# Performance work log

Measured on AMD Instinct MI355X. Metric: run time of the kernel, lower is better.

## Reference

```python
import jax, jax.numpy as jnp
import numpy as np

VOCAB = 100000
EMBED = 300
BATCH = 131072
NEG = 10


def setup_inputs() -> dict:
    key = jax.random.key(0)
    k1, k2, k3, k4, k5 = jax.random.split(key, 5)
    center_words = jax.random.randint(k1, (BATCH,), 0, VOCAB)
    context_words = jax.random.randint(k2, (BATCH,), 0, VOCAB)
    neg_samples = jax.random.randint(k3, (BATCH, NEG), 0, VOCAB)
    in_embed = jax.random.normal(k4, (VOCAB, EMBED), dtype=jnp.float32)
    out_embed = jax.random.normal(k5, (VOCAB, EMBED), dtype=jnp.float32)
    return {
        "center_words": center_words,
        "context_words": context_words,
        "neg_samples": neg_samples,
        "in_embed": in_embed,
        "out_embed": out_embed,
    }


def reference(center_words, context_words, neg_samples, in_embed, out_embed):
    center_e = in_embed[center_words]          # [B, D]
    context_e = out_embed[context_words]       # [B, D]
    neg_e = out_embed[neg_samples]             # [B, K, D]
    pos_scores = jnp.sum(center_e * context_e, axis=1)            # [B]
    neg_scores = jnp.einsum("bkd,bd->bk", neg_e, center_e)        # [B, K]
    pos_loss = jax.nn.log_sigmoid(pos_scores)                      # [B]
    neg_loss = jnp.sum(jax.nn.log_sigmoid(-neg_scores), axis=1)   # [B]
    return -jnp.mean(pos_loss + neg_loss)
```

## Files before the change

### kernel.cpp

```cpp
#include <hip/hip_runtime.h>
#include <math.h>

#define VOCABN 100000
#define EMBED 300
#define BATCH 131072
#define NEG 10
#define RQ 19
#define NWORDS (VOCABN * EMBED)

typedef float float2v __attribute__((ext_vector_type(2)));


template <bool HI>
__device__ __forceinline__ float2v cvt2(unsigned int w) {
    return __builtin_amdgcn_cvt_pk_f32_fp8((int)w, HI);
}
template <bool HI>
__device__ __forceinline__ unsigned int pk2(unsigned int old, float a, float b) {
    return (unsigned int)__builtin_amdgcn_cvt_pk_fp8_f32(a, b, (int)old, HI);
}

__device__ __forceinline__ float dqf(const float* c, uint4 q) {
    float2v p;
    float s = 0.0f;
    p = cvt2<false>(q.x); s += c[0]  * p.x + c[1]  * p.y;
    p = cvt2<true >(q.x); s += c[2]  * p.x + c[3]  * p.y;
    p = cvt2<false>(q.y); s += c[4]  * p.x + c[5]  * p.y;
    p = cvt2<true >(q.y); s += c[6]  * p.x + c[7]  * p.y;
    p = cvt2<false>(q.z); s += c[8]  * p.x + c[9]  * p.y;
    p = cvt2<true >(q.z); s += c[10] * p.x + c[11] * p.y;
    p = cvt2<false>(q.w); s += c[12] * p.x + c[13] * p.y;
    p = cvt2<true >(q.w); s += c[14] * p.x + c[15] * p.y;
    return s;
}

__device__ __forceinline__ void unp16(uint4 q, float* f) {
    float2v p;
    p = cvt2<false>(q.x); f[0]  = p.x; f[1]  = p.y;
    p = cvt2<true >(q.x); f[2]  = p.x; f[3]  = p.y;
    p = cvt2<false>(q.y); f[4]  = p.x; f[5]  = p.y;
    p = cvt2<true >(q.y); f[6]  = p.x; f[7]  = p.y;
    p = cvt2<false>(q.z); f[8]  = p.x; f[9]  = p.y;
    p = cvt2<true >(q.z); f[10] = p.x; f[11] = p.y;
    p = cvt2<false>(q.w); f[12] = p.x; f[13] = p.y;
    p = cvt2<true >(q.w); f[14] = p.x; f[15] = p.y;
}


__device__ __forceinline__ float dot4(const float4 a, const float4 b) {
    return a.x * b.x + a.y * b.y + a.z * b.z + a.w * b.w;
}

__device__ __forceinline__ float lsig(float x) {
    float ax = fabsf(x);
    return fminf(x, 0.0f) - __logf(1.0f + __expf(-ax));
}

__device__ __forceinline__ float reduce16(float v) {
    v += __shfl_xor(v, 1);
    v += __shfl_xor(v, 2);
    v += __shfl_xor(v, 4);
    v += __shfl_xor(v, 8);
    return v;
}

__global__ void sgns_zero_acc(double* acc) { *acc = 0.0; }

__global__ void sgns_finalize(const double* __restrict__ acc, float* __restrict__ out) {
    *out = (float)(-(*acc) / (double)BATCH);
}


__global__ __launch_bounds__(256) void cvt_fp8(const float* __restrict__ src,
                                               uint4* __restrict__ dst, int nrows) {
    const int total = nrows * RQ;
    const int stride = gridDim.x * blockDim.x;
    for (int i = blockIdx.x * blockDim.x + threadIdx.x; i < total; i += stride) {
        int r = i / RQ;
        int q = i - r * RQ;
        const float4* s = reinterpret_cast<const float4*>(src + (size_t)r * EMBED + q * 16);
        float4 a = s[0], b = s[1], c = s[2];
        float4 d = make_float4(0.f, 0.f, 0.f, 0.f);
        if (q != RQ - 1) d = s[3];
        uint4 o;
        unsigned int w;
        w = pk2<false>(0, a.x, a.y); o.x = pk2<true>(w, a.z, a.w);
        w = pk2<false>(0, b.x, b.y); o.y = pk2<true>(w, b.z, b.w);
        w = pk2<false>(0, c.x, c.y); o.z = pk2<true>(w, c.z, c.w);
        w = pk2<false>(0, d.x, d.y); o.w = pk2<true>(w, d.z, d.w);
        dst[i] = o;
    }
}


__global__ __launch_bounds__(256) void sgns_fp8(
    const int* __restrict__ center_words,
    const int* __restrict__ context_words,
    const int* __restrict__ neg_samples,
    const uint4* __restrict__ inQ,
    const uint4* __restrict__ outQ,
    double* __restrict__ acc)
{
    const int lane = threadIdx.x & 15;
    const int group = (blockIdx.x * blockDim.x + threadIdx.x) >> 4;
    const int nGroups = (gridDim.x * blockDim.x) >> 4;
    const int tl = (lane < 3) ? lane : 0;
    const float tmask = (lane < 3) ? 1.0f : 0.0f;

    float tsum = 0.0f;

    for (int b = group; b < BATCH; b += nGroups) {
        const int cw = center_words[b];
        const int xw = context_words[b];
        const int2* np = reinterpret_cast<const int2*>(neg_samples + (size_t)b * NEG);
        int2 q0 = np[0], q1 = np[1], q2 = np[2], q3 = np[3], q4 = np[4];
        int idx[11] = {xw, q0.x, q0.y, q1.x, q1.y, q2.x, q2.y, q3.x, q3.y, q4.x, q4.y};

        const uint4* cp = inQ + (size_t)cw * RQ;
        uint4 cm = cp[lane];
        uint4 ct = cp[16 + tl];
        float cf[32];
        unp16(cm, cf);
        unp16(ct, cf + 16);
        #pragma unroll
        for (int j = 16; j < 32; ++j) cf[j] *= tmask;

        float part[11];
        uint4 bm[3], bt[3];
        {
            const uint4* p0 = outQ + (size_t)idx[0] * RQ;
            bm[0] = p0[lane]; bt[0] = p0[16 + tl];
            const uint4* p1 = outQ + (size_t)idx[1] * RQ;
            bm[1] = p1[lane]; bt[1] = p1[16 + tl];
        }
        #pragma unroll
        for (int j = 0; j < 11; ++j) {
            if (j + 2 < 11) {
                const uint4* p = outQ + (size_t)idx[j + 2] * RQ;
                bm[(j + 2) % 3] = p[lane];
                bt[(j + 2) % 3] = p[16 + tl];
            }
            part[j] = dqf(cf, bm[j % 3]) + dqf(cf + 16, bt[j % 3]);
        }

        #pragma unroll
        for (int j = 0; j < 11; ++j) part[j] = reduce16(part[j]);

        float loss = lsig(part[0]);
        #pragma unroll
        for (int j = 1; j < 11; ++j) loss += lsig(-part[j]);

        tsum += (lane == 0) ? loss : 0.0f;
    }

    float w = tsum;
    #pragma unroll
    for (int m = 1; m < 64; m <<= 1) w += __shfl_xor(w, m);

    __shared__ double ssum[4];
    const int wid = threadIdx.x >> 6;
    if ((threadIdx.x & 63) == 0) ssum[wid] = (double)w;
    __syncthreads();
    if (threadIdx.x == 0) {
        atomicAdd(acc, ssum[0] + ssum[1] + ssum[2] + ssum[3]);
    }
}


__global__ __launch_bounds__(256) void sgns_f32(
    const int* __restrict__ center_words,
    const int* __restrict__ context_words,
    const int* __restrict__ neg_samples,
    const float* __restrict__ in_embed,
    const float* __restrict__ out_embed,
    double* __restrict__ acc)
{
    const int lane = threadIdx.x & 15;
    const int group = (blockIdx.x * blockDim.x + threadIdx.x) >> 4;
    const int nGroups = (gridDim.x * blockDim.x) >> 4;

    const float4* inE = reinterpret_cast<const float4*>(in_embed);
    const float4* outE = reinterpret_cast<const float4*>(out_embed);
    const int RU = EMBED / 4;
    const int TAIL = RU - 64;

    float tsum = 0.0f;

    for (int b = group; b < BATCH; b += nGroups) {
        const int c = center_words[b];
        const int ctx = context_words[b];

        const float4* crow = inE + (size_t)c * RU;
        float4 c0 = crow[lane + 0];
        float4 c1 = crow[lane + 16];
        float4 c2 = crow[lane + 32];
        float4 c3 = crow[lane + 48];
        float4 c4 = make_float4(0.f, 0.f, 0.f, 0.f);
        if (lane < TAIL) c4 = crow[lane + 64];

        const float4* xrow = outE + (size_t)ctx * RU;
        float p = dot4(c0, xrow[lane + 0])
                + dot4(c1, xrow[lane + 16])
                + dot4(c2, xrow[lane + 32])
                + dot4(c3, xrow[lane + 48]);
        if (lane < TAIL) p += dot4(c4, xrow[lane + 64]);
        p = reduce16(p);

        float loss = lsig(p);

        #pragma unroll
        for (int k = 0; k < NEG; ++k) {
            const int nk = neg_samples[b * NEG + k];
            const float4* nrow = outE + (size_t)nk * RU;
            float s = dot4(c0, nrow[lane + 0])
                    + dot4(c1, nrow[lane + 16])
                    + dot4(c2, nrow[lane + 32])
                    + dot4(c3, nrow[lane + 48]);
            if (lane < TAIL) s += dot4(c4, nrow[lane + 64]);
            s = reduce16(s);
            loss += lsig(-s);
        }

        tsum += (lane == 0) ? loss : 0.0f;
    }

    float w = tsum;
    #pragma unroll
    for (int m = 1; m < 64; m <<= 1) w += __shfl_xor(w, m);

    __shared__ double ssum[4];
    const int wid = threadIdx.x >> 6;
    if ((threadIdx.x & 63) == 0) ssum[wid] = (double)w;
    __syncthreads();
    if (threadIdx.x == 0) {
        atomicAdd(acc, ssum[0] + ssum[1] + ssum[2] + ssum[3]);
    }
}


extern "C" void kernel_launch(void* const* d_in, const int* in_sizes, int n_in,
                              void* d_out, int out_size, void* d_ws, size_t ws_size,
                              hipStream_t stream) {
    const int* center = (const int*)d_in[0];
    const int* context = (const int*)d_in[1];
    const int* negs = (const int*)d_in[2];
    const float* inE = (const float*)d_in[3];
    const float* outE = (const float*)d_in[4];
    float* out = (float*)d_out;
    double* acc = (double*)d_ws;

    sgns_zero_acc<<<1, 1, 0, stream>>>(acc);

    const size_t TBL_BYTES = (size_t)VOCABN * RQ * 16;
    const size_t need = 256 + 2 * TBL_BYTES;

    if (ws_size >= need) {
        uint4* inQ = (uint4*)((char*)d_ws + 256);
        uint4* outQ = (uint4*)((char*)d_ws + 256 + TBL_BYTES);
        cvt_fp8<<<4096, 256, 0, stream>>>(inE, inQ, VOCABN);
        cvt_fp8<<<4096, 256, 0, stream>>>(outE, outQ, VOCABN);
        sgns_fp8<<<2048, 256, 0, stream>>>(center, context, negs,
                                           (const uint4*)inQ, (const uint4*)outQ, acc);
    } else {
        sgns_f32<<<2048, 256, 0, stream>>>(center, context, negs, inE, outE, acc);
    }

    sgns_finalize<<<1, 1, 0, stream>>>(acc, out);
}
```

Baseline: 153.8 us.

## Merge fp8 table conversions, pad rows to 20 chunks, use packed float2 math

Fuses the two table-to-fp8 conversion launches into one kernel using nontemporal loads, and pads each quantized row to 20 16-byte chunks so row starts align and the tail read uses four lanes. The dot product is rewritten to use packed float2 multiply-accumulate. The aim is to cut launch overhead, cache pollution during conversion, and ALU work in the gather-dot loop. The workspace need grows because of the padding.

```diff
diff --git a/kernel.cpp b/kernel.cpp
--- a/kernel.cpp
+++ b/kernel.cpp
@@ -5,10 +5,10 @@
 #define EMBED 300
 #define BATCH 131072
 #define NEG 10
-#define RQ 19
-#define NWORDS (VOCABN * EMBED)
+#define RQ 20
 
 typedef float float2v __attribute__((ext_vector_type(2)));
+typedef float float4v __attribute__((ext_vector_type(4)));
 
 
 template <bool HI>
@@ -20,30 +20,27 @@
     return (unsigned int)__builtin_amdgcn_cvt_pk_fp8_f32(a, b, (int)old, HI);
 }
 
-__device__ __forceinline__ float dqf(const float* c, uint4 q) {
-    float2v p;
-    float s = 0.0f;
-    p = cvt2<false>(q.x); s += c[0]  * p.x + c[1]  * p.y;
-    p = cvt2<true >(q.x); s += c[2]  * p.x + c[3]  * p.y;
-    p = cvt2<false>(q.y); s += c[4]  * p.x + c[5]  * p.y;
-    p = cvt2<true >(q.y); s += c[6]  * p.x + c[7]  * p.y;
-    p = cvt2<false>(q.z); s += c[8]  * p.x + c[9]  * p.y;
-    p = cvt2<true >(q.z); s += c[10] * p.x + c[11] * p.y;
-    p = cvt2<false>(q.w); s += c[12] * p.x + c[13] * p.y;
-    p = cvt2<true >(q.w); s += c[14] * p.x + c[15] * p.y;
-    return s;
-}
-
-__device__ __forceinline__ void unp16(uint4 q, float* f) {
-    float2v p;
-    p = cvt2<false>(q.x); f[0]  = p.x; f[1]  = p.y;
-    p = cvt2<true >(q.x); f[2]  = p.x; f[3]  = p.y;
-    p = cvt2<false>(q.y); f[4]  = p.x; f[5]  = p.y;
-    p = cvt2<true >(q.y); f[6]  = p.x; f[7]  = p.y;
-    p = cvt2<false>(q.z); f[8]  = p.x; f[9]  = p.y;
-    p = cvt2<true >(q.z); f[10] = p.x; f[11] = p.y;
-    p = cvt2<false>(q.w); f[12] = p.x; f[13] = p.y;
-    p = cvt2<true >(q.w); f[14] = p.x; f[15] = p.y;
+__device__ __forceinline__ float2v dq8(const float2v* c, uint4 q, float2v acc) {
+    acc += c[0] * cvt2<false>(q.x);
+    acc += c[1] * cvt2<true >(q.x);
+    acc += c[2] * cvt2<false>(q.y);
+    acc += c[3] * cvt2<true >(q.y);
+    acc += c[4] * cvt2<false>(q.z);
+    acc += c[5] * cvt2<true >(q.z);
+    acc += c[6] * cvt2<false>(q.w);
+    acc += c[7] * cvt2<true >(q.w);
+    return acc;
+}
+
+__device__ __forceinline__ void unp8(uint4 q, float2v* f) {
+    f[0] = cvt2<false>(q.x);
+    f[1] = cvt2<true >(q.x);
+    f[2] = cvt2<false>(q.y);
+    f[3] = cvt2<true >(q.y);
+    f[4] = cvt2<false>(q.z);
+    f[5] = cvt2<true >(q.z);
+    f[6] = cvt2<false>(q.w);
+    f[7] = cvt2<true >(q.w);
 }
 
 
@@ -71,24 +68,36 @@
 }
 
 
-__global__ __launch_bounds__(256) void cvt_fp8(const float* __restrict__ src,
-                                               uint4* __restrict__ dst, int nrows) {
-    const int total = nrows * RQ;
+__global__ __launch_bounds__(256) void cvt_fp8_all(
+    const float* __restrict__ srcA, const float* __restrict__ srcB,
+    uint4* __restrict__ dstA, uint4* __restrict__ dstB)
+{
+    const int T = VOCABN * RQ;
+    const int total = 2 * T;
     const int stride = gridDim.x * blockDim.x;
     for (int i = blockIdx.x * blockDim.x + threadIdx.x; i < total; i += stride) {
-        int r = i / RQ;
-        int q = i - r * RQ;
-        const float4* s = reinterpret_cast<const float4*>(src + (size_t)r * EMBED + q * 16);
-        float4 a = s[0], b = s[1], c = s[2];
-        float4 d = make_float4(0.f, 0.f, 0.f, 0.f);
-        if (q != RQ - 1) d = s[3];
-        uint4 o;
-        unsigned int w;
-        w = pk2<false>(0, a.x, a.y); o.x = pk2<true>(w, a.z, a.w);
-        w = pk2<false>(0, b.x, b.y); o.y = pk2<true>(w, b.z, b.w);
-        w = pk2<false>(0, c.x, c.y); o.z = pk2<true>(w, c.z, c.w);
-        w = pk2<false>(0, d.x, d.y); o.w = pk2<true>(w, d.z, d.w);
-        dst[i] = o;
+        const int t = (i >= T);
+        const int j = i - t * T;
+        const int r = j / RQ;
+        const int q = j - r * RQ;
+        const float* src = t ? srcB : srcA;
+        uint4* dst = t ? dstB : dstA;
+
+        uint4 o = make_uint4(0u, 0u, 0u, 0u);
+        if (q < 19) {
+            const float4v* s = reinterpret_cast<const float4v*>(src + (size_t)r * EMBED + q * 16);
+            float4v a = __builtin_nontemporal_load(s);
+            float4v b = __builtin_nontemporal_load(s + 1);
+            float4v c = __builtin_nontemporal_load(s + 2);
+            float4v d = {0.f, 0.f, 0.f, 0.f};
+            if (q < 18) d = __builtin_nontemporal_load(s + 3);
+            unsigned int w;
+            w = pk2<false>(0, a[0], a[1]); o.x = pk2<true>(w, a[2], a[3]);
+            w = pk2<false>(0, b[0], b[1]); o.y = pk2<true>(w, b[2], b[3]);
+            w = pk2<false>(0, c[0], c[1]); o.z = pk2<true>(w, c[2], c[3]);
+            w = pk2<false>(0, d[0], d[1]); o.w = pk2<true>(w, d[2], d[3]);
+        }
+        dst[(size_t)t * 0 + j + (size_t)0] = o;
     }
 }
 
@@ -104,8 +113,8 @@
     const int lane = threadIdx.x & 15;
     const int group = (blockIdx.x * blockDim.x + threadIdx.x) >> 4;
     const int nGroups = (gridDim.x * blockDim.x) >> 4;
-    const int tl = (lane < 3) ? lane : 0;
-    const float tmask = (lane < 3) ? 1.0f : 0.0f;
+    const int tq = 16 + (lane & 3);
+    const float tmask = (lane < 4) ? 1.0f : 0.0f;
 
     float tsum = 0.0f;
 
@@ -118,29 +127,31 @@
 
         const uint4* cp = inQ + (size_t)cw * RQ;
         uint4 cm = cp[lane];
-        uint4 ct = cp[16 + tl];
-        float cf[32];
-        unp16(cm, cf);
-        unp16(ct, cf + 16);
-        #pragma unroll
-        for (int j = 16; j < 32; ++j) cf[j] *= tmask;
+        uint4 ct = cp[tq];
+        float2v cf2[16];
+        unp8(cm, cf2);
+        unp8(ct, cf2 + 8);
+        #pragma unroll
+        for (int j = 8; j < 16; ++j) cf2[j] *= tmask;
 
         float part[11];
         uint4 bm[3], bt[3];
         {
             const uint4* p0 = outQ + (size_t)idx[0] * RQ;
-            bm[0] = p0[lane]; bt[0] = p0[16 + tl];
+            bm[0] = p0[lane]; bt[0] = p0[tq];
             const uint4* p1 = outQ + (size_t)idx[1] * RQ;
-            bm[1] = p1[lane]; bt[1] = p1[16 + tl];
+            bm[1] = p1[lane]; bt[1] = p1[tq];
         }
         #pragma unroll
         for (int j = 0; j < 11; ++j) {
             if (j + 2 < 11) {
                 const uint4* p = outQ + (size_t)idx[j + 2] * RQ;
                 bm[(j + 2) % 3] = p[lane];
-                bt[(j + 2) % 3] = p[16 + tl];
+                bt[(j + 2) % 3] = p[tq];
             }
-            part[j] = dqf(cf, bm[j % 3]) + dqf(cf + 16, bt[j % 3]);
+            float2v a2 = dq8(cf2, bm[j % 3], (float2v){0.f, 0.f});
+            a2 = dq8(cf2 + 8, bt[j % 3], a2);
+            part[j] = a2.x + a2.y;
         }
 
         #pragma unroll
@@ -257,8 +268,7 @@
     if (ws_size >= need) {
         uint4* inQ = (uint4*)((char*)d_ws + 256);
         uint4* outQ = (uint4*)((char*)d_ws + 256 + TBL_BYTES);
-        cvt_fp8<<<4096, 256, 0, stream>>>(inE, inQ, VOCABN);
-        cvt_fp8<<<4096, 256, 0, stream>>>(outE, outQ, VOCABN);
+        cvt_fp8_all<<<4096, 256, 0, stream>>>(inE, outE, inQ, outQ);
         sgns_fp8<<<2048, 256, 0, stream>>>(center, context, negs,
                                            (const uint4*)inQ, (const uint4*)outQ, acc);
     } else {
```

New measurement: 198.2 us. 1.29x slower.
